# Optimization experiments

Hardware: AMD Instinct MI355X
Metric: run time of the kernel (lower is better)

Reference implementation:

```python
import jax, jax.numpy as jnp
import numpy as np

N_NODES = 100000
N_NBRS = 16
D_IN = 512
D_EGO = 32
D_LOCAL = 32
D_GLOBAL = 32


def setup_inputs() -> dict:
    key = jax.random.key(0)
    ks = jax.random.split(key, 12)
    x = jax.random.uniform(ks[0], (N_NODES, D_IN), dtype=jnp.float32)
    # adj_list: row 0 = source (neighbor) node, row 1 = destination node.
    # score_local_sparse reshapes to [N, n, d_local], so dst must be each node
    # index repeated N_NBRS times, in order.
    src = jax.random.randint(ks[1], (N_NODES * N_NBRS,), 0, N_NODES, dtype=jnp.int32)
    dst = jnp.repeat(jnp.arange(N_NODES, dtype=jnp.int32), N_NBRS)
    adj_list = jnp.stack([src, dst], axis=0)
    return {
        "adj_list": adj_list,
        "x": x,
        "qk_ego_w": jax.random.normal(ks[2], (D_EGO, D_IN), dtype=jnp.float32) * 0.04,
        "v_ego_w": jax.random.normal(ks[3], (D_IN, D_EGO), dtype=jnp.float32) - 2.0,
        "q_local_w": jax.random.normal(ks[4], (D_LOCAL, D_IN), dtype=jnp.float32) / 10.0 - 2.0,
        "k_local_w": jax.random.normal(ks[5], (D_LOCAL, D_IN), dtype=jnp.float32) / 10.0 - 2.0,
        "v_local_w": jax.random.normal(ks[6], (D_IN, D_LOCAL), dtype=jnp.float32) / 10.0 - 2.0,
        "q_global_w": jax.random.normal(ks[7], (D_GLOBAL, D_IN), dtype=jnp.float32) / 10.0 - 2.0,
        "k_global_w": jax.random.normal(ks[8], (D_GLOBAL, D_IN), dtype=jnp.float32) / 10.0 - 2.0,
        "v_global_w": jax.random.normal(ks[9], (D_IN, D_GLOBAL), dtype=jnp.float32) / 10.0 - 2.0,
        "bias_b": jnp.zeros((1, D_IN), dtype=jnp.float32),
    }


def _nonneg(w):
    return jax.nn.elu(w) + 1.0


def _norm_nonneg(w):
    t = jax.nn.sigmoid(w)
    return t / t.sum()


def reference(adj_list, x, qk_ego_w, v_ego_w, q_local_w, k_local_w, v_local_w,
              q_global_w, k_global_w, v_global_w, bias_b):
    n_cells, d_in = x.shape
    inv = 1.0 / d_in
    inv2 = inv * inv

    # ego branch: plain linear, squared scores
    ego_emb = x @ qk_ego_w.T                      # [N, d_ego]
    ego_scores = (ego_emb * inv) ** 2             # [N, d_ego]

    # local branch: gather-based bilinear scores over k-NN graph
    q_loc = x @ _norm_nonneg(q_local_w).T         # [N, d_local]
    k_loc = x @ _nonneg(k_local_w).T              # [N, d_local]
    prod = q_loc[adj_list[1]] * k_loc[adj_list[0]]  # [E, d_local]
    n_nbr = prod.shape[0] // n_cells
    local_scores = prod.reshape(n_cells, n_nbr, -1) * inv2  # [N, n, d_local]
    exp_local = local_scores.sum(axis=1)          # [N, d_local] (sum over neighbors)

    # global branch: bilinear with mean cell x_bar
    x_bar = x.mean(axis=0, keepdims=True)         # [1, d_in]
    q_glob = x @ _norm_nonneg(q_global_w).T       # [N, d_global]
    k_glob = x_bar @ _nonneg(k_global_w).T        # [1, d_global]
    exp_global = q_glob * k_glob * inv2           # [N, d_global]

    sum_exp = (0.001
               + ego_scores.sum(axis=-1, keepdims=True)
               + exp_local.sum(axis=-1, keepdims=True)
               + exp_global.sum(axis=-1, keepdims=True))  # [N, 1]

    ego_res = (ego_scores / sum_exp) @ _nonneg(v_ego_w).T       # [N, d_out]
    local_res = (exp_local / sum_exp) @ _nonneg(v_local_w).T    # [N, d_out]
    global_res = (exp_global / sum_exp) @ _nonneg(v_global_w).T # [N, d_out]

    res = ego_res + local_res + global_res + (jax.nn.elu(bias_b) + 1.0)
    return res
```

## Files before the change

kernel.cpp:

```cpp
#include <hip/hip_runtime.h>
#include <hip/hip_bf16.h>
#include <math.h>

#define NNODES 100000
#define NNBRS  16
#define NBLK   ((NNODES + 127) / 128)
#define KRA    ((NBLK + 7) / 8)

typedef short  s16x8 __attribute__((ext_vector_type(8)));
typedef ushort u16x8 __attribute__((ext_vector_type(8)));
typedef float  f32x4 __attribute__((ext_vector_type(4)));

__device__ __forceinline__ float nonneg_(float w) { return w > 0.f ? w + 1.f : __expf(w); }
__device__ __forceinline__ float sigmoid_(float w) { return 1.f / (1.f + __expf(-w)); }
__device__ __forceinline__ ushort f2b(float f) {
    unsigned u = __builtin_bit_cast(unsigned, f);
    return (ushort)((u + 0x7FFFu + ((u >> 16) & 1u)) >> 16);
}
__device__ __forceinline__ float b2f(ushort h) {
    return __builtin_bit_cast(float, (unsigned)h << 16);
}
__device__ __forceinline__ short fbh(float f) {
    __hip_bfloat16 h = __float2bfloat16(f);
    return __builtin_bit_cast(short, h);
}
__device__ __forceinline__ s16x8 cvt8(float4 lo, float4 hi) {
    s16x8 r;
    r[0] = fbh(lo.x); r[1] = fbh(lo.y); r[2] = fbh(lo.z); r[3] = fbh(lo.w);
    r[4] = fbh(hi.x); r[5] = fbh(hi.y); r[6] = fbh(hi.z); r[7] = fbh(hi.w);
    return r;
}

#define BAR() do {                                             \
    __builtin_amdgcn_sched_barrier(0);                         \
    asm volatile("s_waitcnt lgkmcnt(0)" ::: "memory");         \
    __builtin_amdgcn_sched_barrier(0);                         \
    __builtin_amdgcn_s_barrier();                              \
    __builtin_amdgcn_sched_barrier(0);                         \
} while (0)

__global__ __launch_bounds__(256) void k_sumsig(const float* __restrict__ qlw,
                                                const float* __restrict__ qgw,
                                                float* __restrict__ sums) {
    __shared__ float rr[8];
    const int tid = threadIdx.x, lane = tid & 63, wv = tid >> 6;
    const int base = blockIdx.x * 512;
    float s0 = sigmoid_(qlw[base + tid]) + sigmoid_(qlw[base + 256 + tid]);
    float s1 = sigmoid_(qgw[base + tid]) + sigmoid_(qgw[base + 256 + tid]);
#pragma unroll
    for (int o = 32; o > 0; o >>= 1) {
        s0 += __shfl_down(s0, o);
        s1 += __shfl_down(s1, o);
    }
    if (lane == 0) { rr[wv] = s0; rr[4 + wv] = s1; }
    __syncthreads();
    if (tid == 0) atomicAdd(&sums[0], rr[0] + rr[1] + rr[2] + rr[3]);
    if (tid == 1) atomicAdd(&sums[1], rr[4] + rr[5] + rr[6] + rr[7]);
}

__global__ __launch_bounds__(256) void k_prep(const float* __restrict__ qk_ego,
                                              const float* __restrict__ qlw,
                                              const float* __restrict__ klw,
                                              const float* __restrict__ qgw,
                                              const float* __restrict__ ve,
                                              const float* __restrict__ vl,
                                              const float* __restrict__ vg,
                                              const float* __restrict__ bias_b,
                                              ushort* __restrict__ B1t,
                                              ushort* __restrict__ Vt,
                                              float* __restrict__ biasvec) {
    int idx = blockIdx.x * 256 + threadIdx.x;
    if (idx < 128 * 512) {
        int o = idx >> 9, k = idx & 511;
        float v;
        if (o < 32)       v = qk_ego[o * 512 + k];
        else if (o < 64)  v = sigmoid_(qlw[(o - 32) * 512 + k]);
        else if (o < 96)  v = nonneg_(klw[(o - 64) * 512 + k]);
        else              v = sigmoid_(qgw[(o - 96) * 512 + k]);
        B1t[idx] = f2b(v);
    } else if (idx < 128 * 512 + 512 * 96) {
        int j = idx - 128 * 512;
        int d = j / 96, e = j % 96;
        const float* src = (e < 32) ? ve : (e < 64 ? vl : vg);
        Vt[j] = f2b(nonneg_(src[d * 32 + (e & 31)]));
    } else if (idx < 128 * 512 + 512 * 96 + 512) {
        int d = idx - 128 * 512 - 512 * 96;
        float b = bias_b[d];
        biasvec[d] = (b > 0.f ? b + 1.f : __expf(b));
    }
}

__global__ __launch_bounds__(512, 2) void k_projx(const float* __restrict__ x,
                                                  const ushort* __restrict__ B1t,
                                                  ushort* __restrict__ ego_a,
                                                  ushort* __restrict__ qloc_a,
                                                  ushort* __restrict__ kloc_a,
                                                  ushort* __restrict__ qglob_a,
                                                  float* __restrict__ xcs) {
    __shared__ ushort As[128 * 128];
    __shared__ ushort Bs[128 * 128];
    __shared__ float  cs[8][512];
    const int t = threadIdx.x, lane = t & 63, w = t >> 6;
    const int lr = lane & 15, g = lane >> 4;
    const int row0 = blockIdx.x * 128;
    const int arow_ = t >> 4;
    const int acol_ = (t & 15) * 8;
    const char* B1tc = (const char*)B1t;

    uint4 bst[4];
#define BLOAD(seg) { _Pragma("unroll")                                        \
    for (int c = 0; c < 4; c++) {                                             \
        int l = c * 512 + t; int r = l >> 4; int sl = l & 15;                 \
        bst[c] = *(const uint4*)(B1tc + r * 1024 + (seg) * 256 + sl * 16);    \
    } }
#define BWRITE() { _Pragma("unroll")                                          \
    for (int c = 0; c < 4; c++) {                                             \
        int l = c * 512 + t; int r = l >> 4; int sl = l & 15;                 \
        *(uint4*)((char*)Bs + r * 256 + ((sl * 16) ^ ((r & 7) << 4))) =       \
            bst[c];                                                           \
    } }

    float4 al0[4], al1[4];
#define ALOAD(seg) { _Pragma("unroll")                                        \
    for (int p = 0; p < 4; p++) {                                             \
        int rr = p * 32 + arow_;                                              \
        int grow = row0 + rr; if (grow > NNODES - 1) grow = NNODES - 1;       \
        const float* sp = x + (size_t)grow * 512 + (seg) * 128 + acol_;       \
        al0[p] = *(const float4*)(sp);                                        \
        al1[p] = *(const float4*)(sp + 4);                                    \
    } }
#define AWRITE(seg) {                                                         \
    float a8[8] = {0.f,0.f,0.f,0.f,0.f,0.f,0.f,0.f};                          \
    _Pragma("unroll")                                                         \
    for (int p = 0; p < 4; p++) {                                             \
        int rr = p * 32 + arow_;                                              \
        if (row0 + rr < NNODES) {                                             \
            a8[0]+=al0[p].x; a8[1]+=al0[p].y; a8[2]+=al0[p].z; a8[3]+=al0[p].w;\
            a8[4]+=al1[p].x; a8[5]+=al1[p].y; a8[6]+=al1[p].z; a8[7]+=al1[p].w;\
        }                                                                     \
        *(s16x8*)((char*)As + rr * 256 + ((acol_ * 2) ^ ((rr & 7) << 4))) =   \
            cvt8(al0[p], al1[p]);                                             \
    }                                                                         \
    _Pragma("unroll")                                                         \
    for (int j = 0; j < 8; j++) {                                             \
        a8[j] += __shfl_xor(a8[j], 16);                                       \
        a8[j] += __shfl_xor(a8[j], 32);                                       \
    }                                                                         \
    if ((lane >> 4) == 0) { _Pragma("unroll")                                 \
        for (int j = 0; j < 8; j++)                                           \
            cs[w][(seg) * 128 + lr * 8 + j] = a8[j];                          \
    } }

    f32x4 acc[8];
#pragma unroll
    for (int n = 0; n < 8; n++) acc[n] = (f32x4){0.f, 0.f, 0.f, 0.f};

    ALOAD(0)
    BLOAD(0)
    AWRITE(0)
    BWRITE()
    BAR();

#pragma unroll
    for (int seg = 0; seg < 4; seg++) {
        if (seg < 3) { ALOAD(seg + 1) BLOAD(seg + 1) }
#pragma unroll
        for (int st = 0; st < 4; st++) {
            const int ar = w * 16 + lr;
            s16x8 af = *(const s16x8*)((const char*)As + ar * 256 +
                                       ((st * 64 + g * 16) ^ ((ar & 7) << 4)));
#pragma unroll
            for (int n = 0; n < 8; n++) {
                s16x8 bf = *(const s16x8*)((const char*)Bs + (n * 16 + lr) * 256 +
                                           ((st * 64 + g * 16) ^ ((lr & 7) << 4)));
                acc[n] = __builtin_amdgcn_mfma_f32_16x16x32_bf16(af, bf, acc[n], 0, 0, 0);
            }
        }
        if (seg < 3) {
            BAR();
            AWRITE(seg + 1)
            BWRITE()
            BAR();
        }
    }
#undef ALOAD
#undef AWRITE
#undef BLOAD
#undef BWRITE

    __syncthreads();
    if (t < 512) {
        float s = cs[0][t] + cs[1][t] + cs[2][t] + cs[3][t]
                + cs[4][t] + cs[5][t] + cs[6][t] + cs[7][t];
        xcs[(size_t)blockIdx.x * 512 + t] = s;
    }
    char* regn = (char*)Bs + w * 4096;
#pragma unroll
    for (int n = 0; n < 8; n++) {
        const int col = (n >> 1) * 32 + (n & 1) * 16 + lr;
#pragma unroll
        for (int i = 0; i < 4; i++) {
            int row = g * 4 + i;
            *(ushort*)(regn + row * 256 + ((col * 2) ^ ((row & 7) << 4))) =
                f2b(acc[n][i]);
        }
    }
    {
        const int rr = lane & 15, a2 = lane >> 4;
        uint4 v0 = *(const uint4*)(regn + rr * 256 + (( 0 + a2 * 64) ^ ((rr & 7) << 4)));
        uint4 v1 = *(const uint4*)(regn + rr * 256 + ((16 + a2 * 64) ^ ((rr & 7) << 4)));
        uint4 v2 = *(const uint4*)(regn + rr * 256 + ((32 + a2 * 64) ^ ((rr & 7) << 4)));
        uint4 v3 = *(const uint4*)(regn + rr * 256 + ((48 + a2 * 64) ^ ((rr & 7) << 4)));
        int grow = row0 + w * 16 + rr;
        if (grow < NNODES) {
            ushort* ap = (a2 == 0) ? ego_a : (a2 == 1) ? qloc_a
                        : (a2 == 2) ? kloc_a : qglob_a;
            uint4* dp = (uint4*)(ap + (size_t)grow * 32);
            dp[0] = v0; dp[1] = v1; dp[2] = v2; dp[3] = v3;
        }
    }
}

__global__ __launch_bounds__(256) void k_kredA(const float* __restrict__ xcs,
                                               float* __restrict__ csum2) {
    const int t = threadIdx.x, b = blockIdx.x;
    float s1 = 0.f, s2 = 0.f;
#pragma unroll
    for (int r = 0; r < 8; r++) {
        int row = b * 8 + r;
        if (row < NBLK) {
            s1 += xcs[(size_t)row * 512 + t];
            s2 += xcs[(size_t)row * 512 + 256 + t];
        }
    }
    csum2[(size_t)b * 512 + t] = s1;
    csum2[(size_t)b * 512 + 256 + t] = s2;
}

__global__ __launch_bounds__(256) void k_kredB(const float* __restrict__ csum2,
                                               const float* __restrict__ kgw,
                                               float* __restrict__ kacc) {
    __shared__ float cs[512];
    const int t = threadIdx.x;
    float s0 = 0.f, s1 = 0.f;
    for (int b = 0; b < KRA; b++) {
        s0 += csum2[(size_t)b * 512 + t];
        s1 += csum2[(size_t)b * 512 + 256 + t];
    }
    cs[t] = s0; cs[256 + t] = s1;
    __syncthreads();
    const int e = t >> 3, j = t & 7;
    float p = 0.f;
    for (int d = j * 64; d < j * 64 + 64; d++)
        p += cs[d] * nonneg_(kgw[e * 512 + d]);
    p += __shfl_xor(p, 1);
    p += __shfl_xor(p, 2);
    p += __shfl_xor(p, 4);
    if (j == 0) kacc[e] = p;
}

__global__ __launch_bounds__(256, 4) void k_fused(const ushort* __restrict__ ego_a,
                                                  const ushort* __restrict__ qloc_a,
                                                  const ushort* __restrict__ kloc_a,
                                                  const ushort* __restrict__ qglob_a,
                                                  const int* __restrict__ src,
                                                  const float* __restrict__ kacc,
                                                  const float* __restrict__ sums,
                                                  const ushort* __restrict__ Vt,
                                                  const float* __restrict__ biasvec,
                                                  float* __restrict__ out) {
    __shared__ float4 stg4[2048];
    char* stg = (char*)stg4;
    const int t = threadIdx.x, lane = t & 63, w = t >> 6;
    const int lr = lane & 15, g = lane >> 4;
    const int node = blockIdx.x * 64 + w * 16 + lr;
    const int nc = node < NNODES ? node : NNODES - 1;

    const float inv = 1.f / 512.f;
    const float inv2 = inv * inv;
    const float scl = inv2 / sums[0];
    const float scg = inv2 / sums[1] * (1.f / (float)NNODES);
    float kg[8];
    {
        float4 kg0 = *(const float4*)(kacc + g * 8);
        float4 kg1 = *(const float4*)(kacc + g * 8 + 4);
        kg[0]=kg0.x; kg[1]=kg0.y; kg[2]=kg0.z; kg[3]=kg0.w;
        kg[4]=kg1.x; kg[5]=kg1.y; kg[6]=kg1.z; kg[7]=kg1.w;
    }

    s16x8 p0, p1, p2;
    {
        u16x8 e8 = *(const u16x8*)(ego_a   + (size_t)nc * 32 + g * 8);
        u16x8 q8 = *(const u16x8*)(qloc_a  + (size_t)nc * 32 + g * 8);
        u16x8 g8 = *(const u16x8*)(qglob_a + (size_t)nc * 32 + g * 8);
        int4 si0 = *(const int4*)(src + (size_t)nc * 16);
        int4 si1 = *(const int4*)(src + (size_t)nc * 16 + 4);
        int4 si2 = *(const int4*)(src + (size_t)nc * 16 + 8);
        int4 si3 = *(const int4*)(src + (size_t)nc * 16 + 12);
        float ks[8] = {0.f,0.f,0.f,0.f,0.f,0.f,0.f,0.f};
#define GAT(sn) {                                                             \
        u16x8 kv = *(const u16x8*)(kloc_a + (size_t)(sn) * 32 + g * 8);       \
        _Pragma("unroll")                                                     \
        for (int j = 0; j < 8; j++) ks[j] += b2f(kv[j]);                      \
    }
        GAT(si0.x) GAT(si0.y) GAT(si0.z) GAT(si0.w)
        GAT(si1.x) GAT(si1.y) GAT(si1.z) GAT(si1.w)
        GAT(si2.x) GAT(si2.y) GAT(si2.z) GAT(si2.w)
        GAT(si3.x) GAT(si3.y) GAT(si3.z) GAT(si3.w)
#undef GAT
        float se[8], sl[8], sg[8];
        float tt = 0.f;
#pragma unroll
        for (int j = 0; j < 8; j++) {
            float e = b2f(e8[j]) * inv;
            se[j] = e * e;
            sl[j] = b2f(q8[j]) * ks[j] * scl;
            sg[j] = b2f(g8[j]) * kg[j] * scg;
            tt += se[j] + sl[j] + sg[j];
        }
        tt += __shfl_xor(tt, 16);
        tt += __shfl_xor(tt, 32);
        float is = 1.f / (0.001f + tt);
#pragma unroll
        for (int j = 0; j < 8; j++) {
            p0[j] = (short)f2b(se[j] * is);
            p1[j] = (short)f2b(sl[j] * is);
            p2[j] = (short)f2b(sg[j] * is);
        }
    }

    const int srow = w * 16 + lr;
    const int sxor = (srow & 7) << 4;
#pragma unroll
    for (int gi = 0; gi < 4; gi++) {
        if (gi) __syncthreads();
#pragma unroll
        for (int m2 = 0; m2 < 8; m2++) {
            const int m = gi * 8 + m2;
            const ushort* vp = Vt + (size_t)(m * 16 + lr) * 96 + g * 8;
            s16x8 a0 = *(const s16x8*)(vp);
            s16x8 a1 = *(const s16x8*)(vp + 32);
            s16x8 a2 = *(const s16x8*)(vp + 64);
            f32x4 dA = (f32x4){0.f,0.f,0.f,0.f};
            dA = __builtin_amdgcn_mfma_f32_16x16x32_bf16(a0, p0, dA, 0, 0, 0);
            dA = __builtin_amdgcn_mfma_f32_16x16x32_bf16(a1, p1, dA, 0, 0, 0);
            dA = __builtin_amdgcn_mfma_f32_16x16x32_bf16(a2, p2, dA, 0, 0, 0);
            float4 bb = *(const float4*)(biasvec + m * 16 + g * 4);
            float4 o4 = {dA[0]+bb.x, dA[1]+bb.y, dA[2]+bb.z, dA[3]+bb.w};
            *(float4*)(stg + srow * 512 + ((m2 * 64 + g * 16) ^ sxor)) = o4;
        }
        __syncthreads();
#pragma unroll
        for (int k = 0; k < 8; k++) {
            const int lin = k * 1024 + t * 4;
            const int row = lin >> 7, inrow = lin & 127;
            f32x4 v = *(const f32x4*)(stg + row * 512 +
                                      ((inrow * 4) ^ ((row & 7) << 4)));
            const int gnode = blockIdx.x * 64 + row;
            if (gnode < NNODES)
                __builtin_nontemporal_store(
                    v, (f32x4*)(out + (size_t)gnode * 512 + gi * 128 + inrow));
        }
    }
}

extern "C" void kernel_launch(void* const* d_in, const int* in_sizes, int n_in,
                              void* d_out, int out_size, void* d_ws, size_t ws_size,
                              hipStream_t stream) {
    (void)in_sizes; (void)n_in; (void)out_size; (void)ws_size;
    const int*   adj    = (const int*)d_in[0];
    const float* x      = (const float*)d_in[1];
    const float* qk_ego = (const float*)d_in[2];
    const float* v_ego  = (const float*)d_in[3];
    const float* qlw    = (const float*)d_in[4];
    const float* klw    = (const float*)d_in[5];
    const float* vl     = (const float*)d_in[6];
    const float* qgw    = (const float*)d_in[7];
    const float* kgw    = (const float*)d_in[8];
    const float* vg     = (const float*)d_in[9];
    const float* bias_b = (const float*)d_in[10];
    float* out = (float*)d_out;
    float* ws  = (float*)d_ws;

    float*  kacc    = ws;
    float*  sums    = ws + 32;
    float*  biasvec = ws + 64;
    ushort* B1t     = (ushort*)(ws + 1024);
    ushort* Vt      = (ushort*)(ws + 33792);
    ushort* ego_a   = (ushort*)(ws + 65536);
    ushort* qloc_a  = (ushort*)(ws + 65536 + 1600000);
    ushort* kloc_a  = (ushort*)(ws + 65536 + 3200000);
    ushort* qglob_a = (ushort*)(ws + 65536 + 4800000);
    float*  xcs     = ws + 6465536;
    float*  csum2   = ws + 6465536 + 400384;

    (void)hipMemsetAsync(sums, 0, 2 * sizeof(float), stream);
    k_sumsig<<<32, 256, 0, stream>>>(qlw, qgw, sums);
    {
        int total = 128 * 512 + 512 * 96 + 512;
        k_prep<<<(total + 255) / 256, 256, 0, stream>>>(qk_ego, qlw, klw, qgw,
                                                        v_ego, vl, vg, bias_b,
                                                        B1t, Vt, biasvec);
    }
    k_projx<<<NBLK, 512, 0, stream>>>(x, B1t, ego_a, qloc_a, kloc_a, qglob_a, xcs);
    k_kredA<<<KRA, 256, 0, stream>>>(xcs, csum2);
    k_kredB<<<1, 256, 0, stream>>>(csum2, kgw, kacc);
    k_fused<<<(NNODES + 63) / 64, 256, 0, stream>>>(ego_a, qloc_a, kloc_a, qglob_a,
                                                    adj, kacc, sums, Vt, biasvec, out);
}
```

Measured before the change: 162.2 us.

## Preload each wave's full x rows into bf16 registers upfront in projection kernel

```diff
diff --git a/kernel.cpp b/kernel.cpp
--- a/kernel.cpp
+++ b/kernel.cpp
@@ -90,7 +90,7 @@
     }
 }
 
-__global__ __launch_bounds__(512, 2) void k_projx(const float* __restrict__ x,
+__global__ __launch_bounds__(512, 4) void k_projx(const float* __restrict__ x,
                                                   const ushort* __restrict__ B1t,
                                                   ushort* __restrict__ ego_a,
                                                   ushort* __restrict__ qloc_a,
@@ -103,8 +103,6 @@
     const int t = threadIdx.x, lane = t & 63, w = t >> 6;
     const int lr = lane & 15, g = lane >> 4;
     const int row0 = blockIdx.x * 128;
-    const int arow_ = t >> 4;
-    const int acol_ = (t & 15) * 8;
     const char* B1tc = (const char*)B1t;
 
     uint4 bst[4];
@@ -119,43 +117,46 @@
         *(uint4*)((char*)Bs + r * 256 + ((sl * 16) ^ ((r & 7) << 4))) =       \
             bst[c];                                                           \
     } }
-
-    float4 al0[4], al1[4];
-#define ALOAD(seg) { _Pragma("unroll")                                        \
-    for (int p = 0; p < 4; p++) {                                             \
-        int rr = p * 32 + arow_;                                              \
-        int grow = row0 + rr; if (grow > NNODES - 1) grow = NNODES - 1;       \
-        const float* sp = x + (size_t)grow * 512 + (seg) * 128 + acol_;       \
-        al0[p] = *(const float4*)(sp);                                        \
-        al1[p] = *(const float4*)(sp + 4);                                    \
-    } }
 #define AWRITE(seg) {                                                         \
-    float a8[8] = {0.f,0.f,0.f,0.f,0.f,0.f,0.f,0.f};                          \
-    _Pragma("unroll")                                                         \
-    for (int p = 0; p < 4; p++) {                                             \
-        int rr = p * 32 + arow_;                                              \
-        if (row0 + rr < NNODES) {                                             \
-            a8[0]+=al0[p].x; a8[1]+=al0[p].y; a8[2]+=al0[p].z; a8[3]+=al0[p].w;\
-            a8[4]+=al1[p].x; a8[5]+=al1[p].y; a8[6]+=al1[p].z; a8[7]+=al1[p].w;\
-        }                                                                     \
-        *(s16x8*)((char*)As + rr * 256 + ((acol_ * 2) ^ ((rr & 7) << 4))) =   \
-            cvt8(al0[p], al1[p]);                                             \
-    }                                                                         \
-    _Pragma("unroll")                                                         \
-    for (int j = 0; j < 8; j++) {                                             \
-        a8[j] += __shfl_xor(a8[j], 16);                                       \
-        a8[j] += __shfl_xor(a8[j], 32);                                       \
-    }                                                                         \
-    if ((lane >> 4) == 0) { _Pragma("unroll")                                 \
-        for (int j = 0; j < 8; j++)                                           \
-            cs[w][(seg) * 128 + lr * 8 + j] = a8[j];                          \
-    } }
+    if ((lane >> 4) == (seg)) {                                               \
+        _Pragma("unroll")                                                     \
+        for (int r = 0; r < 16; r++) {                                        \
+            const int rr = w * 16 + r;                                        \
+            *(s16x8*)((char*)As + rr * 256 +                                  \
+                      (((lane & 15) * 16) ^ ((rr & 7) << 4))) = xh[r];        \
+        } } }
+
+    s16x8 xh[16];
+    {
+        float a8[8] = {0.f,0.f,0.f,0.f,0.f,0.f,0.f,0.f};
+#pragma unroll
+        for (int r4 = 0; r4 < 16; r4 += 4) {
+            float4 tl[4], th[4];
+#pragma unroll
+            for (int q = 0; q < 4; q++) {
+                int grow = row0 + w * 16 + r4 + q;
+                if (grow > NNODES - 1) grow = NNODES - 1;
+                const float* sp = x + (size_t)grow * 512 + lane * 8;
+                tl[q] = *(const float4*)(sp);
+                th[q] = *(const float4*)(sp + 4);
+            }
+#pragma unroll
+            for (int q = 0; q < 4; q++) {
+                xh[r4 + q] = cvt8(tl[q], th[q]);
+                if (row0 + w * 16 + r4 + q < NNODES) {
+                    a8[0]+=tl[q].x; a8[1]+=tl[q].y; a8[2]+=tl[q].z; a8[3]+=tl[q].w;
+                    a8[4]+=th[q].x; a8[5]+=th[q].y; a8[6]+=th[q].z; a8[7]+=th[q].w;
+                }
+            }
+        }
+#pragma unroll
+        for (int j = 0; j < 8; j++) cs[w][lane * 8 + j] = a8[j];
+    }
 
     f32x4 acc[8];
 #pragma unroll
     for (int n = 0; n < 8; n++) acc[n] = (f32x4){0.f, 0.f, 0.f, 0.f};
 
-    ALOAD(0)
     BLOAD(0)
     AWRITE(0)
     BWRITE()
@@ -163,7 +164,7 @@
 
 #pragma unroll
     for (int seg = 0; seg < 4; seg++) {
-        if (seg < 3) { ALOAD(seg + 1) BLOAD(seg + 1) }
+        if (seg < 3) BLOAD(seg + 1)
 #pragma unroll
         for (int st = 0; st < 4; st++) {
             const int ar = w * 16 + lr;
@@ -183,16 +184,15 @@
             BAR();
         }
     }
-#undef ALOAD
 #undef AWRITE
 #undef BLOAD
 #undef BWRITE
 
     __syncthreads();
-    if (t < 512) {
-        float s = cs[0][t] + cs[1][t] + cs[2][t] + cs[3][t]
-                + cs[4][t] + cs[5][t] + cs[6][t] + cs[7][t];
-        xcs[(size_t)blockIdx.x * 512 + t] = s;
+    {
+        float s = cs[0][t & 511] + cs[1][t & 511] + cs[2][t & 511] + cs[3][t & 511]
+                + cs[4][t & 511] + cs[5][t & 511] + cs[6][t & 511] + cs[7][t & 511];
+        xcs[(size_t)blockIdx.x * 512 + (t & 511)] = s;
     }
     char* regn = (char*)Bs + w * 4096;
 #pragma unroll
```

Measured after the change: 189.8 us. 1.17x slower.
